# Optimization experiments

Hardware: AMD Instinct MI355X
Metric: run time of the kernel (lower is better)

## Reference

```python
import jax, jax.numpy as jnp
import numpy as np

B, IN, OUT, GD, TD, H, W, L = 16, 512, 256, 256, 256, 32, 32, 32
EPS_BN = 1e-5


def _conv2d(x, w, pad):
    return jax.lax.conv_general_dilated(
        x, w, window_strides=(1, 1), padding=[(pad, pad), (pad, pad)],
        dimension_numbers=("NCHW", "OIHW", "NCHW"))


def _up2(x):
    return jnp.repeat(jnp.repeat(x, 2, axis=2), 2, axis=3)


def _l2n(v):  # F.normalize(p=2, dim=1), eps=1e-12
    n = jnp.sqrt(jnp.sum(v * v, axis=1, keepdims=True))
    return v / jnp.maximum(n, 1e-12)


def _context(img_embs, words_embs, mask):
    i = _l2n(img_embs)            # [B, TD, P]
    wd = _l2n(words_embs)         # [B, TD, L]
    sim = jnp.einsum("bcp,bcl->bpl", i, wd)
    sim = jnp.where(mask[:, None, :], -jnp.inf, sim)
    attn = jax.nn.softmax(sim, axis=-1)
    return jnp.einsum("bpl,bcl->bcp", attn, wd)  # [B, TD, P]


def _bn(x, w, b):  # training-mode BatchNorm2d, biased variance
    m = jnp.mean(x, axis=(0, 2, 3), keepdims=True)
    v = jnp.var(x, axis=(0, 2, 3), keepdims=True)
    return (x - m) * jax.lax.rsqrt(v + EPS_BN) * w[None, :, None, None] + b[None, :, None, None]


def setup_inputs():
    key = jax.random.key(0)
    ks = jax.random.split(key, 16)
    s = 0.02
    COND = GD + TD
    return {
        "x": jax.random.normal(ks[0], (B, IN, H, W), jnp.float32),
        "global_cond": jax.random.normal(ks[1], (B, GD), jnp.float32),
        "words_embs": jax.random.normal(ks[2], (B, TD, L), jnp.float32),
        "mask": jax.random.randint(ks[3], (B, L), 0, 2).astype(bool),
        "w_img1": jax.random.normal(ks[4], (TD, IN), jnp.float32) * s,
        "w_img2": jax.random.normal(ks[5], (TD, OUT), jnp.float32) * s,
        "w_c1": jax.random.normal(ks[6], (OUT, IN, 3, 3), jnp.float32) * s,
        "w_c2": jax.random.normal(ks[7], (OUT, OUT, 3, 3), jnp.float32) * s,
        "bn1_w": jnp.ones((IN,), jnp.float32),
        "bn1_b": jnp.zeros((IN,), jnp.float32),
        "bn2_w": jnp.ones((OUT,), jnp.float32),
        "bn2_b": jnp.zeros((OUT,), jnp.float32),
        "w_g1": jax.random.normal(ks[8], (IN, COND), jnp.float32) * s,
        "b_g1": jnp.zeros((IN,), jnp.float32),
        "w_b1": jax.random.normal(ks[9], (IN, COND), jnp.float32) * s,
        "b_b1": jnp.zeros((IN,), jnp.float32),
        "w_g2": jax.random.normal(ks[10], (OUT, COND), jnp.float32) * s,
        "b_g2": jnp.zeros((OUT,), jnp.float32),
        "w_b2": jax.random.normal(ks[11], (OUT, COND), jnp.float32) * s,
        "b_b2": jnp.zeros((OUT,), jnp.float32),
        "w_sc": jax.random.normal(ks[12], (OUT, IN, 1, 1), jnp.float32) * s,
        "b_sc": jnp.zeros((OUT,), jnp.float32),
    }


def reference(x, global_cond, words_embs, mask,
              w_img1, w_img2, w_c1, w_c2,
              bn1_w, bn1_b, bn2_w, bn2_b,
              w_g1, b_g1, w_b1, b_b1,
              w_g2, b_g2, w_b2, b_b2,
              w_sc, b_sc):
    # ---- residual path, stage 1 ----
    img1 = jnp.einsum("tc,bcp->btp", w_img1, x.reshape(B, IN, H * W))
    ctx1 = _context(img1, words_embs, mask)                 # [B, TD, H*W]
    gc = jnp.broadcast_to(global_cond[:, :, None], (B, GD, H * W))
    cond1 = jnp.concatenate([gc, ctx1], axis=1)             # [B, GD+TD, H*W]
    gamma1 = jnp.einsum("oc,bcp->bop", w_g1, cond1) + b_g1[None, :, None]
    beta1 = jnp.einsum("oc,bcp->bop", w_b1, cond1) + b_b1[None, :, None]
    out = gamma1.reshape(B, IN, H, W) * _bn(x, bn1_w, bn1_b) + beta1.reshape(B, IN, H, W)
    out = jax.nn.relu(out)
    out = _up2(out)                                         # [B, IN, 2H, 2W]
    out = _conv2d(out, w_c1, 1)                             # [B, OUT, 2H, 2W]
    h2, w2 = 2 * H, 2 * W
    # ---- residual path, stage 2 ----
    img2 = jnp.einsum("tc,bcp->btp", w_img2, out.reshape(B, OUT, h2 * w2))
    ctx2 = _context(img2, words_embs, mask)                 # [B, TD, h2*w2]
    gc2 = jnp.broadcast_to(global_cond[:, :, None], (B, GD, h2 * w2))
    cond2 = jnp.concatenate([gc2, ctx2], axis=1)
    gamma2 = jnp.einsum("oc,bcp->bop", w_g2, cond2) + b_g2[None, :, None]
    beta2 = jnp.einsum("oc,bcp->bop", w_b2, cond2) + b_b2[None, :, None]
    out = gamma2.reshape(B, OUT, h2, w2) * _bn(out, bn2_w, bn2_b) + beta2.reshape(B, OUT, h2, w2)
    out = jax.nn.relu(out)
    out = _conv2d(out, w_c2, 1)
    # ---- shortcut ----
    sc = _conv2d(_up2(x), w_sc, 0) + b_sc[None, :, None, None]
    return out + sc
```

## Files before the change

kernel.cpp:

```cpp
#include <hip/hip_runtime.h>
#include <hip/hip_bf16.h>
#include <math.h>

#define NB 16
#define CIN1 512
#define COUT 256
#define GD 256
#define TD 256
#define LL 32
#define P1 1024
#define P2 4096
#define CONDC 512

typedef __attribute__((ext_vector_type(8))) short bf16x8;
typedef __attribute__((ext_vector_type(4))) float f32x4;
typedef unsigned short u16;

__device__ __forceinline__ u16 f2b(float f) {
  __hip_bfloat16 h = __float2bfloat16(f);
  return *(u16*)&h;
}

__global__ void bn_stats_kernel(const float* __restrict__ x, float* __restrict__ mean,
                                float* __restrict__ rstd, int C, int HW) {
  int c = blockIdx.x, t = threadIdx.x;
  float s = 0.f, sq = 0.f;
  for (int b = 0; b < NB; ++b) {
    const float* p = x + ((size_t)b * C + c) * HW;
    for (int i = t; i < HW; i += 256) { float v = p[i]; s += v; sq += v * v; }
  }
  __shared__ float ss[256], sq2[256];
  ss[t] = s; sq2[t] = sq; __syncthreads();
  for (int o = 128; o > 0; o >>= 1) {
    if (t < o) { ss[t] += ss[t + o]; sq2[t] += sq2[t + o]; }
    __syncthreads();
  }
  if (t == 0) {
    float n = (float)NB * (float)HW;
    float m = ss[0] / n;
    float v = sq2[0] / n - m * m;
    mean[c] = m;
    rstd[c] = rsqrtf(v + 1e-5f);
  }
}

__global__ void wdn_kernel(const float* __restrict__ we, float* __restrict__ wdn) {
  int b = blockIdx.x >> 5, l = blockIdx.x & 31;
  int t = threadIdx.x;
  const float* base = we + (size_t)b * TD * LL + l;
  float v[4]; float sq = 0.f;
#pragma unroll
  for (int k = 0; k < 4; ++k) { v[k] = base[(size_t)(t * 4 + k) * LL]; sq += v[k] * v[k]; }
#pragma unroll
  for (int o = 32; o > 0; o >>= 1) sq += __shfl_xor(sq, o);
  float r = 1.f / fmaxf(sqrtf(sq), 1e-12f);
  float* ob = wdn + (size_t)b * TD * LL + l;
#pragma unroll
  for (int k = 0; k < 4; ++k) ob[(size_t)(t * 4 + k) * LL] = v[k] * r;
}

__global__ void gvec_kernel(const float* __restrict__ Wg, const float* __restrict__ bias,
                            const float* __restrict__ gc, float* __restrict__ outv, int O) {
  int o = blockIdx.x * 64 + threadIdx.x;
  int b = blockIdx.y;
  if (o >= O) return;
  const float* wr = Wg + (size_t)o * CONDC;
  const float* g = gc + (size_t)b * GD;
  float s = 0.f;
  for (int c = 0; c < GD; ++c) s += wr[c] * g[c];
  outv[(size_t)b * O + o] = s + bias[o];
}

__global__ __launch_bounds__(256) void attnctx_kernel(
    const float* __restrict__ img, const float* __restrict__ wdn,
    const int* __restrict__ mask, float* __restrict__ ctx, int P) {
  __shared__ u16 imgT[64 * 72];
  __shared__ u16 wdnT[32 * 264];
  __shared__ u16 wdnC[256 * 40];
  __shared__ u16 attnB[64 * 40];
  __shared__ float sqP[4][64];
  __shared__ float rnL[64];
  const int b = blockIdx.y, p0 = blockIdx.x * 64;
  const int tid = threadIdx.x;
  const int w = tid >> 6, lane = tid & 63;
  const int l15 = lane & 15, lg = lane >> 4;
  const float* ib = img + (size_t)b * TD * P;
  const float* wb = wdn + (size_t)b * TD * LL;

  for (int i = tid; i < TD * LL; i += 256) {
    int t = i >> 5, l = i & 31;
    u16 v = f2b(wb[i]);
    wdnT[l * 264 + t] = v;
    wdnC[t * 40 + l] = v;
  }

  f32x4 s0 = {}, s1 = {};
  float ssq = 0.f;
  for (int q = 0; q < 4; ++q) {
#pragma unroll
    for (int i = 0; i < 16; i += 2) {
      int t = q * 64 + w * 16 + i;
      float v0 = ib[(size_t)t * P + p0 + lane];
      float v1 = ib[(size_t)(t + 1) * P + p0 + lane];
      ssq += v0 * v0 + v1 * v1;
      unsigned pk = (unsigned)f2b(v0) | ((unsigned)f2b(v1) << 16);
      *(unsigned*)(imgT + lane * 72 + w * 16 + i) = pk;
    }
    __syncthreads();
#pragma unroll
    for (int ks = 0; ks < 2; ++ks) {
      bf16x8 a = *(const bf16x8*)(imgT + (w * 16 + l15) * 72 + ks * 32 + lg * 8);
      bf16x8 b0 = *(const bf16x8*)(wdnT + l15 * 264 + q * 64 + ks * 32 + lg * 8);
      bf16x8 b1 = *(const bf16x8*)(wdnT + (16 + l15) * 264 + q * 64 + ks * 32 + lg * 8);
      s0 = __builtin_amdgcn_mfma_f32_16x16x32_bf16(a, b0, s0, 0, 0, 0);
      s1 = __builtin_amdgcn_mfma_f32_16x16x32_bf16(a, b1, s1, 0, 0, 0);
    }
    __syncthreads();
  }
  sqP[w][lane] = ssq;
  __syncthreads();
  if (tid < 64) {
    float s = sqP[0][tid] + sqP[1][tid] + sqP[2][tid] + sqP[3][tid];
    rnL[tid] = 1.f / fmaxf(sqrtf(s), 1e-12f);
  }
  __syncthreads();
  const bool m0 = mask[b * LL + l15] != 0;
  const bool m1 = mask[b * LL + 16 + l15] != 0;
#pragma unroll
  for (int k = 0; k < 4; ++k) {
    float rn = rnL[w * 16 + lg * 4 + k];
    float v0 = m0 ? -INFINITY : s0[k] * rn;
    float v1 = m1 ? -INFINITY : s1[k] * rn;
    float mx = fmaxf(v0, v1);
#pragma unroll
    for (int o = 1; o < 16; o <<= 1) mx = fmaxf(mx, __shfl_xor(mx, o));
    float e0 = expf(v0 - mx), e1 = expf(v1 - mx);
    float sm = e0 + e1;
#pragma unroll
    for (int o = 1; o < 16; o <<= 1) sm += __shfl_xor(sm, o);
    float inv = 1.f / sm;
    int px = w * 16 + lg * 4 + k;
    attnB[px * 40 + l15] = f2b(e0 * inv);
    attnB[px * 40 + 16 + l15] = f2b(e1 * inv);
  }
  __syncthreads();
  f32x4 acc[4][4] = {};
  bf16x8 bfr[4];
#pragma unroll
  for (int pt = 0; pt < 4; ++pt)
    bfr[pt] = *(const bf16x8*)(attnB + (pt * 16 + l15) * 40 + lg * 8);
#pragma unroll
  for (int cc = 0; cc < 4; ++cc) {
    bf16x8 a = *(const bf16x8*)(wdnC + ((w * 4 + cc) * 16 + l15) * 40 + lg * 8);
#pragma unroll
    for (int pt = 0; pt < 4; ++pt)
      acc[cc][pt] = __builtin_amdgcn_mfma_f32_16x16x32_bf16(a, bfr[pt], acc[cc][pt], 0, 0, 0);
  }
#pragma unroll
  for (int cc = 0; cc < 4; ++cc) {
#pragma unroll
    for (int pt = 0; pt < 4; ++pt) {
#pragma unroll
      for (int k = 0; k < 4; ++k) {
        int c = (w * 4 + cc) * 16 + lg * 4 + k;
        ctx[((size_t)b * TD + c) * P + p0 + pt * 16 + l15] = acc[cc][pt][k];
      }
    }
  }
}

__global__ __launch_bounds__(256, 2) void gemm_mfma_kernel(
    const float* __restrict__ W, int ldw, int c_off,
    const float* __restrict__ X, const float* __restrict__ vec,
    float* __restrict__ Y, int T, int C, int P) {
  __shared__ u16 Wl[2][128 * 44];
  __shared__ u16 Xl[2][128 * 40];
  const int b = blockIdx.z;
  const int t0 = blockIdx.y * 128, p0 = blockIdx.x * 128;
  const int tid = threadIdx.x;
  const int w = tid >> 6, lane = tid & 63;
  const int wo = w >> 1, wq = w & 1;
  const int l15 = lane & 15, lg = lane >> 4;
  const float* Xb = X + (size_t)b * C * P;
  const int wr = tid >> 1, wcH = tid & 1;
  const int xr = tid >> 3, xcG = tid & 7;
  const int csw = xr ^ ((xcG & 3) << 3);
  const float* wsrc = W + (size_t)(t0 + wr) * ldw + c_off + wcH * 16;
  const float* xsrc = Xb + (size_t)xr * P + p0 + xcG * 16;
  const int NK = C / 32;
  f32x4 acc[4][4] = {};
  float4 wreg[4], xreg[4];

#pragma unroll
  for (int j = 0; j < 4; ++j) {
    wreg[j] = *(const float4*)(wsrc + j * 4);
    xreg[j] = *(const float4*)(xsrc + j * 4);
  }
  {
    u16* dst = Wl[0] + wr * 44 + wcH * 16;
#pragma unroll
    for (int j = 0; j < 4; ++j) {
      *(ushort4*)(dst + j * 4) = make_ushort4(f2b(wreg[j].x), f2b(wreg[j].y), f2b(wreg[j].z), f2b(wreg[j].w));
      int px = xcG * 16 + j * 4;
      Xl[0][(px + 0) * 40 + csw] = f2b(xreg[j].x);
      Xl[0][(px + 1) * 40 + csw] = f2b(xreg[j].y);
      Xl[0][(px + 2) * 40 + csw] = f2b(xreg[j].z);
      Xl[0][(px + 3) * 40 + csw] = f2b(xreg[j].w);
    }
  }
  __syncthreads();

  for (int kb = 0; kb < NK; ++kb) {
    const int cur = kb & 1;
    if (kb + 1 < NK) {
      const int c0n = (kb + 1) * 32;
#pragma unroll
      for (int j = 0; j < 4; ++j) {
        wreg[j] = *(const float4*)(wsrc + c0n + j * 4);
        xreg[j] = *(const float4*)(xsrc + (size_t)c0n * P + j * 4);
      }
    }
    bf16x8 a[4], bb[4];
#pragma unroll
    for (int rr = 0; rr < 4; ++rr)
      a[rr] = *(const bf16x8*)(Wl[cur] + (wo * 64 + rr * 16 + l15) * 44 + lg * 8);
#pragma unroll
    for (int ss = 0; ss < 4; ++ss)
      bb[ss] = *(const bf16x8*)(Xl[cur] + (wq * 64 + ss * 16 + l15) * 40 + ((lg ^ ss) << 3));
#pragma unroll
    for (int rr = 0; rr < 4; ++rr)
#pragma unroll
      for (int ss = 0; ss < 4; ++ss)
        acc[rr][ss] = __builtin_amdgcn_mfma_f32_16x16x32_bf16(a[rr], bb[ss], acc[rr][ss], 0, 0, 0);
    if (kb + 1 < NK) {
      const int nxt = cur ^ 1;
      u16* dst = Wl[nxt] + wr * 44 + wcH * 16;
#pragma unroll
      for (int j = 0; j < 4; ++j) {
        *(ushort4*)(dst + j * 4) = make_ushort4(f2b(wreg[j].x), f2b(wreg[j].y), f2b(wreg[j].z), f2b(wreg[j].w));
        int px = xcG * 16 + j * 4;
        Xl[nxt][(px + 0) * 40 + csw] = f2b(xreg[j].x);
        Xl[nxt][(px + 1) * 40 + csw] = f2b(xreg[j].y);
        Xl[nxt][(px + 2) * 40 + csw] = f2b(xreg[j].z);
        Xl[nxt][(px + 3) * 40 + csw] = f2b(xreg[j].w);
      }
      __syncthreads();
    }
  }
#pragma unroll
  for (int rr = 0; rr < 4; ++rr) {
    int tb = t0 + wo * 64 + rr * 16 + lg * 4;
#pragma unroll
    for (int ss = 0; ss < 4; ++ss) {
      int p = p0 + wq * 64 + ss * 16 + l15;
#pragma unroll
      for (int k = 0; k < 4; ++k) {
        int t = tb + k;
        float val = acc[rr][ss][k];
        if (vec) val += vec[(size_t)b * T + t];
        Y[((size_t)b * T + t) * P + p] = val;
      }
    }
  }
}

__global__ __launch_bounds__(256, 2) void gbact_kernel(
    const float* __restrict__ Wg, const float* __restrict__ Wb,
    const float* __restrict__ ctx, const float* __restrict__ gvec,
    const float* __restrict__ bvec, const float* __restrict__ xin,
    const float* __restrict__ mean, const float* __restrict__ rstd,
    const float* __restrict__ bnw, const float* __restrict__ bnb,
    u16* __restrict__ outb, int C, int P) {
  __shared__ u16 shmem[2][16384];
  const int b = blockIdx.z, t0 = blockIdx.y * 128, p0 = blockIdx.x * 128;
  const int tid = threadIdx.x;
  const int w = tid >> 6, lane = tid & 63;
  const int wo = w >> 1, wq = w & 1;
  const int l15 = lane & 15, lg = lane >> 4;
  const float* Xb = ctx + (size_t)b * TD * P;
  const int wr = tid >> 1, wcH = tid & 1;
  const int xr = tid >> 3, xcG = tid & 7;
  const int csw = xr ^ ((xcG & 3) << 3);
  const float* gsrc = Wg + (size_t)(t0 + wr) * CONDC + GD + wcH * 16;
  const float* bsrc = Wb + (size_t)(t0 + wr) * CONDC + GD + wcH * 16;
  const float* xsrc = Xb + (size_t)xr * P + p0 + xcG * 16;
  const int NK = TD / 32;
  f32x4 accg[4][4] = {}, accb[4][4] = {};
  float4 greg[4], breg[4], xreg[4];

#pragma unroll
  for (int j = 0; j < 4; ++j) {
    greg[j] = *(const float4*)(gsrc + j * 4);
    breg[j] = *(const float4*)(bsrc + j * 4);
    xreg[j] = *(const float4*)(xsrc + j * 4);
  }
  {
    u16* dg = shmem[0] + wr * 44 + wcH * 16;
    u16* db = shmem[0] + 5632 + wr * 44 + wcH * 16;
    u16* xl = shmem[0] + 11264;
#pragma unroll
    for (int j = 0; j < 4; ++j) {
      *(ushort4*)(dg + j * 4) = make_ushort4(f2b(greg[j].x), f2b(greg[j].y), f2b(greg[j].z), f2b(greg[j].w));
      *(ushort4*)(db + j * 4) = make_ushort4(f2b(breg[j].x), f2b(breg[j].y), f2b(breg[j].z), f2b(breg[j].w));
      int px = xcG * 16 + j * 4;
      xl[(px + 0) * 40 + csw] = f2b(xreg[j].x);
      xl[(px + 1) * 40 + csw] = f2b(xreg[j].y);
      xl[(px + 2) * 40 + csw] = f2b(xreg[j].z);
      xl[(px + 3) * 40 + csw] = f2b(xreg[j].w);
    }
  }
  __syncthreads();

  for (int kb = 0; kb < NK; ++kb) {
    const int cur = kb & 1;
    if (kb + 1 < NK) {
      const int c0n = (kb + 1) * 32;
#pragma unroll
      for (int j = 0; j < 4; ++j) {
        greg[j] = *(const float4*)(gsrc + c0n + j * 4);
        breg[j] = *(const float4*)(bsrc + c0n + j * 4);
        xreg[j] = *(const float4*)(xsrc + (size_t)c0n * P + j * 4);
      }
    }
    bf16x8 ag[4], ab[4], bb[4];
#pragma unroll
    for (int rr = 0; rr < 4; ++rr) {
      ag[rr] = *(const bf16x8*)(shmem[cur] + (wo * 64 + rr * 16 + l15) * 44 + lg * 8);
      ab[rr] = *(const bf16x8*)(shmem[cur] + 5632 + (wo * 64 + rr * 16 + l15) * 44 + lg * 8);
    }
#pragma unroll
    for (int ss = 0; ss < 4; ++ss)
      bb[ss] = *(const bf16x8*)(shmem[cur] + 11264 + (wq * 64 + ss * 16 + l15) * 40 + ((lg ^ ss) << 3));
#pragma unroll
    for (int rr = 0; rr < 4; ++rr)
#pragma unroll
      for (int ss = 0; ss < 4; ++ss) {
        accg[rr][ss] = __builtin_amdgcn_mfma_f32_16x16x32_bf16(ag[rr], bb[ss], accg[rr][ss], 0, 0, 0);
        accb[rr][ss] = __builtin_amdgcn_mfma_f32_16x16x32_bf16(ab[rr], bb[ss], accb[rr][ss], 0, 0, 0);
      }
    if (kb + 1 < NK) {
      const int nxt = cur ^ 1;
      u16* dg = shmem[nxt] + wr * 44 + wcH * 16;
      u16* db = shmem[nxt] + 5632 + wr * 44 + wcH * 16;
      u16* xl = shmem[nxt] + 11264;
#pragma unroll
      for (int j = 0; j < 4; ++j) {
        *(ushort4*)(dg + j * 4) = make_ushort4(f2b(greg[j].x), f2b(greg[j].y), f2b(greg[j].z), f2b(greg[j].w));
        *(ushort4*)(db + j * 4) = make_ushort4(f2b(breg[j].x), f2b(breg[j].y), f2b(breg[j].z), f2b(breg[j].w));
        int px = xcG * 16 + j * 4;
        xl[(px + 0) * 40 + csw] = f2b(xreg[j].x);
        xl[(px + 1) * 40 + csw] = f2b(xreg[j].y);
        xl[(px + 2) * 40 + csw] = f2b(xreg[j].z);
        xl[(px + 3) * 40 + csw] = f2b(xreg[j].w);
      }
      __syncthreads();
    }
  }
  __syncthreads();
  u16* tbuf = &shmem[0][0];
#pragma unroll
  for (int rr = 0; rr < 4; ++rr) {
    float gv[4], bv[4], mm[4], rs[4], bB[4];
#pragma unroll
    for (int k = 0; k < 4; ++k) {
      int c = t0 + wo * 64 + rr * 16 + lg * 4 + k;
      gv[k] = gvec[(size_t)b * C + c];
      bv[k] = bvec[(size_t)b * C + c];
      mm[k] = mean[c]; rs[k] = rstd[c] * bnw[c]; bB[k] = bnb[c];
    }
#pragma unroll
    for (int ss = 0; ss < 4; ++ss) {
#pragma unroll
      for (int k = 0; k < 4; ++k) {
        int cl = wo * 64 + rr * 16 + lg * 4 + k;
        int pl = wq * 64 + ss * 16 + l15;
        float xv = xin[((size_t)b * C + t0 + cl) * P + p0 + pl];
        float g = accg[rr][ss][k] + gv[k];
        float be = accb[rr][ss][k] + bv[k];
        float val = fmaxf(g * ((xv - mm[k]) * rs[k] + bB[k]) + be, 0.f);
        tbuf[pl * 136 + cl] = f2b(val);
      }
    }
  }
  __syncthreads();
  const int pr = tid >> 1, h = tid & 1;
#pragma unroll
  for (int j = 0; j < 8; ++j) {
    uint4 v = *(uint4*)(tbuf + pr * 136 + h * 64 + j * 8);
    *(uint4*)(outb + ((size_t)b * P + p0 + pr) * C + t0 + h * 64 + j * 8) = v;
  }
}

__global__ void pack_w_kernel(const float* __restrict__ w, u16* __restrict__ wp, int O, int CIN) {
  int lin = blockIdx.x * 256 + threadIdx.x;
  if (lin >= O * CIN) return;
  int o = lin / CIN, c = lin - o * CIN;
  int c0blk = c >> 5, lg = (c >> 3) & 3, cc = c & 7;
  int ot = o >> 4, l15 = o & 15;
  int lane = lg * 16 + l15;
  size_t base = (((size_t)c0blk * (O >> 4) + ot) * 64 + lane) * 8 + cc;
  size_t posStride = (size_t)(CIN >> 5) * (O >> 4) * 512;
  const float* src = w + (size_t)lin * 9;
#pragma unroll
  for (int pos = 0; pos < 9; ++pos)
    wp[pos * posStride + base] = f2b(src[pos]);
}

template <int CIN, bool UP>
__global__ __launch_bounds__(256, 2) void conv_mfma_kernel(
    const u16* __restrict__ Wp, const u16* __restrict__ Xt,
    const float* __restrict__ scs, const float* __restrict__ scb,
    float* __restrict__ Y) {
  constexpr int S = UP ? 32 : 64;
  constexpr int NC0 = CIN >> 5;
  __shared__ u16 Xs[2][4 * 66 * 36];
  const int b = blockIdx.z, pxT = blockIdx.x;
  const int tid = threadIdx.x;
  const int w = tid >> 6, lane = tid & 63;
  const int wo = w >> 1, wp_ = w & 1;
  const int l15 = lane & 15, lg = lane >> 4;
  const int Y0 = pxT * 2;
  const u16* Xb = Xt + (size_t)b * S * S * CIN;
  const size_t posStride = (size_t)NC0 * 16 * 512;
  f32x4 acc[8][4] = {};
  uint2 st[9];

#pragma unroll
  for (int j = 0; j < 9; ++j) {
    int i = tid + j * 256;
    if (i < 2112) {
      int r = i / 528, rem = i - r * 528, col = rem >> 3, ch = rem & 7;
      int uy = Y0 - 1 + r, ux = col - 1;
      uint2 v = make_uint2(0u, 0u);
      if (uy >= 0 && uy < 64 && ux >= 0 && ux < 64) {
        int sy = UP ? (uy >> 1) : uy, sx = UP ? (ux >> 1) : ux;
        v = *(const uint2*)(Xb + ((size_t)sy * S + sx) * CIN + ch * 4);
      }
      st[j] = v;
    }
  }
#pragma unroll
  for (int j = 0; j < 9; ++j) {
    int i = tid + j * 256;
    if (i < 2112) {
      int r = i / 528, rem = i - r * 528, col = rem >> 3, ch = rem & 7;
      *(uint2*)(&Xs[0][(r * 66 + col) * 36 + ch * 4]) = st[j];
    }
  }
  __syncthreads();

  for (int c0b = 0; c0b < NC0; ++c0b) {
    const int cur = c0b & 1;
    if (c0b + 1 < NC0) {
      const int c0n = (c0b + 1) << 5;
#pragma unroll
      for (int j = 0; j < 9; ++j) {
        int i = tid + j * 256;
        if (i < 2112) {
          int r = i / 528, rem = i - r * 528, col = rem >> 3, ch = rem & 7;
          int uy = Y0 - 1 + r, ux = col - 1;
          uint2 v = make_uint2(0u, 0u);
          if (uy >= 0 && uy < 64 && ux >= 0 && ux < 64) {
            int sy = UP ? (uy >> 1) : uy, sx = UP ? (ux >> 1) : ux;
            v = *(const uint2*)(Xb + ((size_t)sy * S + sx) * CIN + c0n + ch * 4);
          }
          st[j] = v;
        }
      }
    }
    {
      const u16* wbB = Wp + ((size_t)c0b * 16 + wo * 8) * 512 + lane * 8;
      bf16x8 aC[8], aN[8];
#pragma unroll
      for (int rr = 0; rr < 8; ++rr)
        aC[rr] = *(const bf16x8*)(wbB + rr * 512);
#pragma unroll
      for (int pos = 0; pos < 9; ++pos) {
        const int ky = pos / 3, kx = pos - ky * 3;
        if (pos < 8) {
          const u16* wbn = wbB + (size_t)(pos + 1) * posStride;
#pragma unroll
          for (int rr = 0; rr < 8; ++rr)
            aN[rr] = *(const bf16x8*)(wbn + rr * 512);
        }
        const int rowb = ((wp_ + ky) * 66 + kx) * 36 + lg * 8;
#pragma unroll
        for (int ss = 0; ss < 4; ++ss) {
          int idx = rowb + (ss * 16 + l15) * 36;
          union { uint2 q[2]; bf16x8 v; } u;
          u.q[0] = *(const uint2*)(&Xs[cur][idx]);
          u.q[1] = *(const uint2*)(&Xs[cur][idx + 4]);
#pragma unroll
          for (int rr = 0; rr < 8; ++rr)
            acc[rr][ss] = __builtin_amdgcn_mfma_f32_16x16x32_bf16(aC[rr], u.v, acc[rr][ss], 0, 0, 0);
        }
#pragma unroll
        for (int rr = 0; rr < 8; ++rr) aC[rr] = aN[rr];
      }
    }
    if (c0b + 1 < NC0) {
#pragma unroll
      for (int j = 0; j < 9; ++j) {
        int i = tid + j * 256;
        if (i < 2112) {
          int r = i / 528, rem = i - r * 528, col = rem >> 3, ch = rem & 7;
          *(uint2*)(&Xs[cur ^ 1][(r * 66 + col) * 36 + ch * 4]) = st[j];
        }
      }
      __syncthreads();
    }
  }
  const int oBase = wo * 128 + lg * 4;
  const int pxBase = pxT * 128 + wp_ * 64 + l15;
#pragma unroll
  for (int rr = 0; rr < 8; ++rr) {
#pragma unroll
    for (int ss = 0; ss < 4; ++ss) {
      int px = pxBase + ss * 16;
#pragma unroll
      for (int k = 0; k < 4; ++k) {
        int o = oBase + rr * 16 + k;
        float val = acc[rr][ss][k];
        if (scs) {
          int gx = px & 63;
          val += scs[((size_t)b * COUT + o) * P1 + pxT * 32 + (gx >> 1)] + scb[o];
        }
        Y[((size_t)b * COUT + o) * 4096 + px] = val;
      }
    }
  }
}

extern "C" void kernel_launch(void* const* d_in, const int* in_sizes, int n_in,
                              void* d_out, int out_size, void* d_ws, size_t ws_size,
                              hipStream_t stream) {
  const float* x      = (const float*)d_in[0];
  const float* gcond  = (const float*)d_in[1];
  const float* wemb   = (const float*)d_in[2];
  const int*   mask   = (const int*)d_in[3];
  const float* w_img1 = (const float*)d_in[4];
  const float* w_img2 = (const float*)d_in[5];
  const float* w_c1   = (const float*)d_in[6];
  const float* w_c2   = (const float*)d_in[7];
  const float* bn1_w  = (const float*)d_in[8];
  const float* bn1_b  = (const float*)d_in[9];
  const float* bn2_w  = (const float*)d_in[10];
  const float* bn2_b  = (const float*)d_in[11];
  const float* w_g1   = (const float*)d_in[12];
  const float* b_g1   = (const float*)d_in[13];
  const float* w_b1   = (const float*)d_in[14];
  const float* b_b1   = (const float*)d_in[15];
  const float* w_g2   = (const float*)d_in[16];
  const float* b_g2   = (const float*)d_in[17];
  const float* w_b2   = (const float*)d_in[18];
  const float* b_b2   = (const float*)d_in[19];
  const float* w_sc   = (const float*)d_in[20];
  const float* b_sc   = (const float*)d_in[21];
  float* out = (float*)d_out;
  float* ws = (float*)d_ws;

  const size_t MF = 16777216;
  float* A  = ws;
  float* Br = ws + MF;
  float* Cr = ws + 2 * MF;
  float* SM = ws + 3 * MF;
  float* wdn   = SM;
  float* mean1 = SM + 131072;
  float* rstd1 = mean1 + 512;
  float* mean2 = rstd1 + 512;
  float* rstd2 = mean2 + 256;
  float* gvec1 = rstd2 + 256;
  float* bvec1 = gvec1 + 8192;
  float* gvec2 = bvec1 + 8192;
  float* bvec2 = gvec2 + 4096;
  float* wsp   = bvec2 + 4096;
  u16* Wp1 = (u16*)wsp;
  u16* Wp2 = (u16*)(wsp + 655360);

  float* img1   = A;
  float* ctx1   = A + 4194304;
  u16*   Xt1    = (u16*)(A + 8388608);
  float* conv1o = Cr;
  float* img2   = Br;
  float* ctx2   = A;
  u16*   Xt2    = (u16*)Br;
  float* scs    = Cr;

  bn_stats_kernel<<<dim3(CIN1), dim3(256), 0, stream>>>(x, mean1, rstd1, CIN1, P1);
  wdn_kernel<<<dim3(NB * LL), dim3(64), 0, stream>>>(wemb, wdn);
  pack_w_kernel<<<dim3(COUT * CIN1 / 256), dim3(256), 0, stream>>>(w_c1, Wp1, COUT, CIN1);
  pack_w_kernel<<<dim3(COUT * COUT / 256), dim3(256), 0, stream>>>(w_c2, Wp2, COUT, COUT);
  gemm_mfma_kernel<<<dim3(P1 / 128, TD / 128, NB), dim3(256), 0, stream>>>(
      w_img1, CIN1, 0, x, nullptr, img1, TD, CIN1, P1);
  attnctx_kernel<<<dim3(P1 / 64, NB), dim3(256), 0, stream>>>(img1, wdn, mask, ctx1, P1);
  gvec_kernel<<<dim3(CIN1 / 64, NB), dim3(64), 0, stream>>>(w_g1, b_g1, gcond, gvec1, CIN1);
  gvec_kernel<<<dim3(CIN1 / 64, NB), dim3(64), 0, stream>>>(w_b1, b_b1, gcond, bvec1, CIN1);
  gbact_kernel<<<dim3(P1 / 128, CIN1 / 128, NB), dim3(256), 0, stream>>>(
      w_g1, w_b1, ctx1, gvec1, bvec1, x, mean1, rstd1, bn1_w, bn1_b, Xt1, CIN1, P1);
  conv_mfma_kernel<CIN1, true><<<dim3(32, 1, NB), dim3(256), 0, stream>>>(
      Wp1, Xt1, nullptr, nullptr, conv1o);

  bn_stats_kernel<<<dim3(COUT), dim3(256), 0, stream>>>(conv1o, mean2, rstd2, COUT, P2);
  gemm_mfma_kernel<<<dim3(P2 / 128, TD / 128, NB), dim3(256), 0, stream>>>(
      w_img2, COUT, 0, conv1o, nullptr, img2, TD, COUT, P2);
  attnctx_kernel<<<dim3(P2 / 64, NB), dim3(256), 0, stream>>>(img2, wdn, mask, ctx2, P2);
  gvec_kernel<<<dim3(COUT / 64, NB), dim3(64), 0, stream>>>(w_g2, b_g2, gcond, gvec2, COUT);
  gvec_kernel<<<dim3(COUT / 64, NB), dim3(64), 0, stream>>>(w_b2, b_b2, gcond, bvec2, COUT);
  gbact_kernel<<<dim3(P2 / 128, COUT / 128, NB), dim3(256), 0, stream>>>(
      w_g2, w_b2, ctx2, gvec2, bvec2, conv1o, mean2, rstd2, bn2_w, bn2_b, Xt2, COUT, P2);
  gemm_mfma_kernel<<<dim3(P1 / 128, COUT / 128, NB), dim3(256), 0, stream>>>(
      w_sc, CIN1, 0, x, nullptr, scs, COUT, CIN1, P1);
  conv_mfma_kernel<COUT, false><<<dim3(32, 1, NB), dim3(256), 0, stream>>>(
      Wp2, Xt2, scs, b_sc, out);
}
```

Measured before the change: 546.4 us.

## Store intermediate activations (img, ctx, conv1 output) in bf16 instead of fp32

The intermediate tensors between kernels (image projections, attention context, first conv output) are now written and read as bf16 rather than fp32. GEMM, attention, gamma/beta and BN-stats kernels are templated to accept bf16 inputs and outputs. The aim is to roughly halve global memory traffic for these large 16x256x4096 buffers and to skip redundant fp32-to-bf16 conversions, since the MFMA paths already consume bf16. In exchange, BN statistics and the elementwise affine now read a rounded conv1 output, which adds precision loss.

```diff
diff --git a/kernel.cpp b/kernel.cpp
--- a/kernel.cpp
+++ b/kernel.cpp
@@ -20,14 +20,24 @@
   __hip_bfloat16 h = __float2bfloat16(f);
   return *(u16*)&h;
 }
-
-__global__ void bn_stats_kernel(const float* __restrict__ x, float* __restrict__ mean,
+__device__ __forceinline__ float b2f(u16 v) {
+  unsigned u = ((unsigned)v) << 16;
+  float f;
+  __builtin_memcpy(&f, &u, 4);
+  return f;
+}
+
+template <bool BF>
+__global__ void bn_stats_kernel(const void* xv, float* __restrict__ mean,
                                 float* __restrict__ rstd, int C, int HW) {
   int c = blockIdx.x, t = threadIdx.x;
   float s = 0.f, sq = 0.f;
   for (int b = 0; b < NB; ++b) {
-    const float* p = x + ((size_t)b * C + c) * HW;
-    for (int i = t; i < HW; i += 256) { float v = p[i]; s += v; sq += v * v; }
+    size_t base = ((size_t)b * C + c) * HW;
+    for (int i = t; i < HW; i += 256) {
+      float v = BF ? b2f(((const u16*)xv)[base + i]) : ((const float*)xv)[base + i];
+      s += v; sq += v * v;
+    }
   }
   __shared__ float ss[256], sq2[256];
   ss[t] = s; sq2[t] = sq; __syncthreads();
@@ -72,8 +82,8 @@
 }
 
 __global__ __launch_bounds__(256) void attnctx_kernel(
-    const float* __restrict__ img, const float* __restrict__ wdn,
-    const int* __restrict__ mask, float* __restrict__ ctx, int P) {
+    const u16* __restrict__ img, const float* __restrict__ wdn,
+    const int* __restrict__ mask, u16* __restrict__ ctx, int P) {
   __shared__ u16 imgT[64 * 72];
   __shared__ u16 wdnT[32 * 264];
   __shared__ u16 wdnC[256 * 40];
@@ -84,7 +94,7 @@
   const int tid = threadIdx.x;
   const int w = tid >> 6, lane = tid & 63;
   const int l15 = lane & 15, lg = lane >> 4;
-  const float* ib = img + (size_t)b * TD * P;
+  const u16* ib = img + (size_t)b * TD * P;
   const float* wb = wdn + (size_t)b * TD * LL;
 
   for (int i = tid; i < TD * LL; i += 256) {
@@ -100,10 +110,11 @@
 #pragma unroll
     for (int i = 0; i < 16; i += 2) {
       int t = q * 64 + w * 16 + i;
-      float v0 = ib[(size_t)t * P + p0 + lane];
-      float v1 = ib[(size_t)(t + 1) * P + p0 + lane];
+      u16 h0 = ib[(size_t)t * P + p0 + lane];
+      u16 h1 = ib[(size_t)(t + 1) * P + p0 + lane];
+      float v0 = b2f(h0), v1 = b2f(h1);
       ssq += v0 * v0 + v1 * v1;
-      unsigned pk = (unsigned)f2b(v0) | ((unsigned)f2b(v1) << 16);
+      unsigned pk = (unsigned)h0 | ((unsigned)h1 << 16);
       *(unsigned*)(imgT + lane * 72 + w * 16 + i) = pk;
     }
     __syncthreads();
@@ -163,16 +174,17 @@
 #pragma unroll
       for (int k = 0; k < 4; ++k) {
         int c = (w * 4 + cc) * 16 + lg * 4 + k;
-        ctx[((size_t)b * TD + c) * P + p0 + pt * 16 + l15] = acc[cc][pt][k];
-      }
-    }
-  }
-}
-
+        ctx[((size_t)b * TD + c) * P + p0 + pt * 16 + l15] = f2b(acc[cc][pt][k]);
+      }
+    }
+  }
+}
+
+template <bool XB, bool YB>
 __global__ __launch_bounds__(256, 2) void gemm_mfma_kernel(
     const float* __restrict__ W, int ldw, int c_off,
-    const float* __restrict__ X, const float* __restrict__ vec,
-    float* __restrict__ Y, int T, int C, int P) {
+    const void* __restrict__ Xv, const float* __restrict__ vec,
+    void* __restrict__ Yv, int T, int C, int P) {
   __shared__ u16 Wl[2][128 * 44];
   __shared__ u16 Xl[2][128 * 40];
   const int b = blockIdx.z;
@@ -181,32 +193,41 @@
   const int w = tid >> 6, lane = tid & 63;
   const int wo = w >> 1, wq = w & 1;
   const int l15 = lane & 15, lg = lane >> 4;
-  const float* Xb = X + (size_t)b * C * P;
   const int wr = tid >> 1, wcH = tid & 1;
   const int xr = tid >> 3, xcG = tid & 7;
   const int csw = xr ^ ((xcG & 3) << 3);
   const float* wsrc = W + (size_t)(t0 + wr) * ldw + c_off + wcH * 16;
-  const float* xsrc = Xb + (size_t)xr * P + p0 + xcG * 16;
+  const float* xsrc32 = XB ? nullptr : (const float*)Xv + (size_t)b * C * P + (size_t)xr * P + p0 + xcG * 16;
+  const u16* xsrc16 = XB ? (const u16*)Xv + (size_t)b * C * P + (size_t)xr * P + p0 + xcG * 16 : nullptr;
   const int NK = C / 32;
   f32x4 acc[4][4] = {};
-  float4 wreg[4], xreg[4];
-
-#pragma unroll
-  for (int j = 0; j < 4; ++j) {
-    wreg[j] = *(const float4*)(wsrc + j * 4);
-    xreg[j] = *(const float4*)(xsrc + j * 4);
+  float4 wreg[4];
+  u16 xst[16];
+
+#pragma unroll
+  for (int j = 0; j < 4; ++j) wreg[j] = *(const float4*)(wsrc + j * 4);
+  if (XB) {
+    union { u16 u[16]; uint4 q[2]; } xu;
+    xu.q[0] = *(const uint4*)(xsrc16);
+    xu.q[1] = *(const uint4*)(xsrc16 + 8);
+#pragma unroll
+    for (int i = 0; i < 16; ++i) xst[i] = xu.u[i];
+  } else {
+#pragma unroll
+    for (int j = 0; j < 4; ++j) {
+      float4 v = *(const float4*)(xsrc32 + j * 4);
+      xst[j * 4 + 0] = f2b(v.x); xst[j * 4 + 1] = f2b(v.y);
+      xst[j * 4 + 2] = f2b(v.z); xst[j * 4 + 3] = f2b(v.w);
+    }
   }
   {
     u16* dst = Wl[0] + wr * 44 + wcH * 16;
 #pragma unroll
-    for (int j = 0; j < 4; ++j) {
+    for (int j = 0; j < 4; ++j)
       *(ushort4*)(dst + j * 4) = make_ushort4(f2b(wreg[j].x), f2b(wreg[j].y), f2b(wreg[j].z), f2b(wreg[j].w));
-      int px = xcG * 16 + j * 4;
-      Xl[0][(px + 0) * 40 + csw] = f2b(xreg[j].x);
-      Xl[0][(px + 1) * 40 + csw] = f2b(xreg[j].y);
-      Xl[0][(px + 2) * 40 + csw] = f2b(xreg[j].z);
-      Xl[0][(px + 3) * 40 + csw] = f2b(xreg[j].w);
-    }
+#pragma unroll
+    for (int i = 0; i < 16; ++i)
+      Xl[0][(xcG * 16 + i) * 40 + csw] = xst[i];
   }
   __syncthreads();
 
@@ -215,9 +236,20 @@
     if (kb + 1 < NK) {
       const int c0n = (kb + 1) * 32;
 #pragma unroll
-      for (int j = 0; j < 4; ++j) {
-        wreg[j] = *(const float4*)(wsrc + c0n + j * 4);
-        xreg[j] = *(const float4*)(xsrc + (size_t)c0n * P + j * 4);
+      for (int j = 0; j < 4; ++j) wreg[j] = *(const float4*)(wsrc + c0n + j * 4);
+      if (XB) {
+        union { u16 u[16]; uint4 q[2]; } xu;
+        xu.q[0] = *(const uint4*)(xsrc16 + (size_t)c0n * P);
+        xu.q[1] = *(const uint4*)(xsrc16 + (size_t)c0n * P + 8);
+#pragma unroll
+        for (int i = 0; i < 16; ++i) xst[i] = xu.u[i];
+      } else {
+#pragma unroll
+        for (int j = 0; j < 4; ++j) {
+          float4 v = *(const float4*)(xsrc32 + (size_t)c0n * P + j * 4);
+          xst[j * 4 + 0] = f2b(v.x); xst[j * 4 + 1] = f2b(v.y);
+          xst[j * 4 + 2] = f2b(v.z); xst[j * 4 + 3] = f2b(v.w);
+        }
       }
     }
     bf16x8 a[4], bb[4];
@@ -236,14 +268,11 @@
       const int nxt = cur ^ 1;
       u16* dst = Wl[nxt] + wr * 44 + wcH * 16;
 #pragma unroll
-      for (int j = 0; j < 4; ++j) {
+      for (int j = 0; j < 4; ++j)
         *(ushort4*)(dst + j * 4) = make_ushort4(f2b(wreg[j].x), f2b(wreg[j].y), f2b(wreg[j].z), f2b(wreg[j].w));
-        int px = xcG * 16 + j * 4;
-        Xl[nxt][(px + 0) * 40 + csw] = f2b(xreg[j].x);
-        Xl[nxt][(px + 1) * 40 + csw] = f2b(xreg[j].y);
-        Xl[nxt][(px + 2) * 40 + csw] = f2b(xreg[j].z);
-        Xl[nxt][(px + 3) * 40 + csw] = f2b(xreg[j].w);
-      }
+#pragma unroll
+      for (int i = 0; i < 16; ++i)
+        Xl[nxt][(xcG * 16 + i) * 40 + csw] = xst[i];
       __syncthreads();
     }
   }
@@ -258,16 +287,18 @@
         int t = tb + k;
         float val = acc[rr][ss][k];
         if (vec) val += vec[(size_t)b * T + t];
-        Y[((size_t)b * T + t) * P + p] = val;
-      }
-    }
-  }
-}
-
+        if (YB) ((u16*)Yv)[((size_t)b * T + t) * P + p] = f2b(val);
+        else    ((float*)Yv)[((size_t)b * T + t) * P + p] = val;
+      }
+    }
+  }
+}
+
+template <bool XINB>
 __global__ __launch_bounds__(256, 2) void gbact_kernel(
     const float* __restrict__ Wg, const float* __restrict__ Wb,
-    const float* __restrict__ ctx, const float* __restrict__ gvec,
-    const float* __restrict__ bvec, const float* __restrict__ xin,
+    const u16* __restrict__ ctx, const float* __restrict__ gvec,
+    const float* __restrict__ bvec, const void* __restrict__ xinv,
     const float* __restrict__ mean, const float* __restrict__ rstd,
     const float* __restrict__ bnw, const float* __restrict__ bnb,
     u16* __restrict__ outb, int C, int P) {
@@ -277,22 +308,28 @@
   const int w = tid >> 6, lane = tid & 63;
   const int wo = w >> 1, wq = w & 1;
   const int l15 = lane & 15, lg = lane >> 4;
-  const float* Xb = ctx + (size_t)b * TD * P;
   const int wr = tid >> 1, wcH = tid & 1;
   const int xr = tid >> 3, xcG = tid & 7;
   const int csw = xr ^ ((xcG & 3) << 3);
   const float* gsrc = Wg + (size_t)(t0 + wr) * CONDC + GD + wcH * 16;
   const float* bsrc = Wb + (size_t)(t0 + wr) * CONDC + GD + wcH * 16;
-  const float* xsrc = Xb + (size_t)xr * P + p0 + xcG * 16;
+  const u16* xsrc = ctx + (size_t)b * TD * P + (size_t)xr * P + p0 + xcG * 16;
   const int NK = TD / 32;
   f32x4 accg[4][4] = {}, accb[4][4] = {};
-  float4 greg[4], breg[4], xreg[4];
+  float4 greg[4], breg[4];
+  u16 xst[16];
 
 #pragma unroll
   for (int j = 0; j < 4; ++j) {
     greg[j] = *(const float4*)(gsrc + j * 4);
     breg[j] = *(const float4*)(bsrc + j * 4);
-    xreg[j] = *(const float4*)(xsrc + j * 4);
+  }
+  {
+    union { u16 u[16]; uint4 q[2]; } xu;
+    xu.q[0] = *(const uint4*)(xsrc);
+    xu.q[1] = *(const uint4*)(xsrc + 8);
+#pragma unroll
+    for (int i = 0; i < 16; ++i) xst[i] = xu.u[i];
   }
   {
     u16* dg = shmem[0] + wr * 44 + wcH * 16;
@@ -302,12 +339,10 @@
     for (int j = 0; j < 4; ++j) {
       *(ushort4*)(dg + j * 4) = make_ushort4(f2b(greg[j].x), f2b(greg[j].y), f2b(greg[j].z), f2b(greg[j].w));
       *(ushort4*)(db + j * 4) = make_ushort4(f2b(breg[j].x), f2b(breg[j].y), f2b(breg[j].z), f2b(breg[j].w));
-      int px = xcG * 16 + j * 4;
-      xl[(px + 0) * 40 + csw] = f2b(xreg[j].x);
-      xl[(px + 1) * 40 + csw] = f2b(xreg[j].y);
-      xl[(px + 2) * 40 + csw] = f2b(xreg[j].z);
-      xl[(px + 3) * 40 + csw] = f2b(xreg[j].w);
-    }
+    }
+#pragma unroll
+    for (int i = 0; i < 16; ++i)
+      xl[(xcG * 16 + i) * 40 + csw] = xst[i];
   }
   __syncthreads();
 
@@ -319,8 +354,12 @@
       for (int j = 0; j < 4; ++j) {
         greg[j] = *(const float4*)(gsrc + c0n + j * 4);
         breg[j] = *(const float4*)(bsrc + c0n + j * 4);
-        xreg[j] = *(const float4*)(xsrc + (size_t)c0n * P + j * 4);
-      }
+      }
+      union { u16 u[16]; uint4 q[2]; } xu;
+      xu.q[0] = *(const uint4*)(xsrc + (size_t)c0n * P);
+      xu.q[1] = *(const uint4*)(xsrc + (size_t)c0n * P + 8);
+#pragma unroll
+      for (int i = 0; i < 16; ++i) xst[i] = xu.u[i];
     }
     bf16x8 ag[4], ab[4], bb[4];
 #pragma unroll
@@ -347,12 +386,10 @@
       for (int j = 0; j < 4; ++j) {
         *(ushort4*)(dg + j * 4) = make_ushort4(f2b(greg[j].x), f2b(greg[j].y), f2b(greg[j].z), f2b(greg[j].w));
         *(ushort4*)(db + j * 4) = make_ushort4(f2b(breg[j].x), f2b(breg[j].y), f2b(breg[j].z), f2b(breg[j].w));
-        int px = xcG * 16 + j * 4;
-        xl[(px + 0) * 40 + csw] = f2b(xreg[j].x);
-        xl[(px + 1) * 40 + csw] = f2b(xreg[j].y);
-        xl[(px + 2) * 40 + csw] = f2b(xreg[j].z);
-        xl[(px + 3) * 40 + csw] = f2b(xreg[j].w);
-      }
+      }
+#pragma unroll
+      for (int i = 0; i < 16; ++i)
+        xl[(xcG * 16 + i) * 40 + csw] = xst[i];
       __syncthreads();
     }
   }
@@ -374,7 +411,8 @@
       for (int k = 0; k < 4; ++k) {
         int cl = wo * 64 + rr * 16 + lg * 4 + k;
         int pl = wq * 64 + ss * 16 + l15;
-        float xv = xin[((size_t)b * C + t0 + cl) * P + p0 + pl];
+        size_t xidx = ((size_t)b * C + t0 + cl) * P + p0 + pl;
+        float xv = XINB ? b2f(((const u16*)xinv)[xidx]) : ((const float*)xinv)[xidx];
         float g = accg[rr][ss][k] + gv[k];
         float be = accb[rr][ss][k] + bv[k];
         float val = fmaxf(g * ((xv - mm[k]) * rs[k] + bB[k]) + be, 0.f);
@@ -406,11 +444,11 @@
     wp[pos * posStride + base] = f2b(src[pos]);
 }
 
-template <int CIN, bool UP>
+template <int CIN, bool UP, bool OUTB>
 __global__ __launch_bounds__(256, 2) void conv_mfma_kernel(
     const u16* __restrict__ Wp, const u16* __restrict__ Xt,
     const float* __restrict__ scs, const float* __restrict__ scb,
-    float* __restrict__ Y) {
+    void* __restrict__ Yv) {
   constexpr int S = UP ? 32 : 64;
   constexpr int NC0 = CIN >> 5;
   __shared__ u16 Xs[2][4 * 66 * 36];
@@ -525,7 +563,8 @@
           int gx = px & 63;
           val += scs[((size_t)b * COUT + o) * P1 + pxT * 32 + (gx >> 1)] + scb[o];
         }
-        Y[((size_t)b * COUT + o) * 4096 + px] = val;
+        if (OUTB) ((u16*)Yv)[((size_t)b * COUT + o) * 4096 + px] = f2b(val);
+        else      ((float*)Yv)[((size_t)b * COUT + o) * 4096 + px] = val;
       }
     }
   }
@@ -577,39 +616,39 @@
   u16* Wp1 = (u16*)wsp;
   u16* Wp2 = (u16*)(wsp + 655360);
 
-  float* img1   = A;
-  float* ctx1   = A + 4194304;
-  u16*   Xt1    = (u16*)(A + 8388608);
-  float* conv1o = Cr;
-  float* img2   = Br;
-  float* ctx2   = A;
-  u16*   Xt2    = (u16*)Br;
-  float* scs    = Cr;
-
-  bn_stats_kernel<<<dim3(CIN1), dim3(256), 0, stream>>>(x, mean1, rstd1, CIN1, P1);
+  u16* img1   = (u16*)A;
+  u16* ctx1   = (u16*)A + 4194304;
+  u16* Xt1    = (u16*)A + 8388608;
+  u16* conv1o = (u16*)Cr;
+  u16* img2   = (u16*)Br;
+  u16* ctx2   = (u16*)A;
+  u16* Xt2    = (u16*)Br;
+  float* scs  = Cr;
+
+  bn_stats_kernel<false><<<dim3(CIN1), dim3(256), 0, stream>>>(x, mean1, rstd1, CIN1, P1);
   wdn_kernel<<<dim3(NB * LL), dim3(64), 0, stream>>>(wemb, wdn);
   pack_w_kernel<<<dim3(COUT * CIN1 / 256), dim3(256), 0, stream>>>(w_c1, Wp1, COUT, CIN1);
   pack_w_kernel<<<dim3(COUT * COUT / 256), dim3(256), 0, stream>>>(w_c2, Wp2, COUT, COUT);
-  gemm_mfma_kernel<<<dim3(P1 / 128, TD / 128, NB), dim3(256), 0, stream>>>(
+  gemm_mfma_kernel<false, true><<<dim3(P1 / 128, TD / 128, NB), dim3(256), 0, stream>>>(
       w_img1, CIN1, 0, x, nullptr, img1, TD, CIN1, P1);
   attnctx_kernel<<<dim3(P1 / 64, NB), dim3(256), 0, stream>>>(img1, wdn, mask, ctx1, P1);
   gvec_kernel<<<dim3(CIN1 / 64, NB), dim3(64), 0, stream>>>(w_g1, b_g1, gcond, gvec1, CIN1);
   gvec_kernel<<<dim3(CIN1 / 64, NB), dim3(64), 0, stream>>>(w_b1, b_b1, gcond, bvec1, CIN1);
-  gbact_kernel<<<dim3(P1 / 128, CIN1 / 128, NB), dim3(256), 0, stream>>>(
+  gbact_kernel<false><<<dim3(P1 / 128, CIN1 / 128, NB), dim3(256), 0, stream>>>(
       w_g1, w_b1, ctx1, gvec1, bvec1, x, mean1, rstd1, bn1_w, bn1_b, Xt1, CIN1, P1);
-  conv_mfma_kernel<CIN1, true><<<dim3(32, 1, NB), dim3(256), 0, stream>>>(
+  conv_mfma_kernel<CIN1, true, true><<<dim3(32, 1, NB), dim3(256), 0, stream>>>(
       Wp1, Xt1, nullptr, nullptr, conv1o);
 
-  bn_stats_kernel<<<dim3(COUT), dim3(256), 0, stream>>>(conv1o, mean2, rstd2, COUT, P2);
-  gemm_mfma_kernel<<<dim3(P2 / 128, TD / 128, NB), dim3(256), 0, stream>>>(
+  bn_stats_kernel<true><<<dim3(COUT), dim3(256), 0, stream>>>(conv1o, mean2, rstd2, COUT, P2);
+  gemm_mfma_kernel<true, true><<<dim3(P2 / 128, TD / 128, NB), dim3(256), 0, stream>>>(
       w_img2, COUT, 0, conv1o, nullptr, img2, TD, COUT, P2);
   attnctx_kernel<<<dim3(P2 / 64, NB), dim3(256), 0, stream>>>(img2, wdn, mask, ctx2, P2);
   gvec_kernel<<<dim3(COUT / 64, NB), dim3(64), 0, stream>>>(w_g2, b_g2, gcond, gvec2, COUT);
   gvec_kernel<<<dim3(COUT / 64, NB), dim3(64), 0, stream>>>(w_b2, b_b2, gcond, bvec2, COUT);
-  gbact_kernel<<<dim3(P2 / 128, COUT / 128, NB), dim3(256), 0, stream>>>(
+  gbact_kernel<true><<<dim3(P2 / 128, COUT / 128, NB), dim3(256), 0, stream>>>(
       w_g2, w_b2, ctx2, gvec2, bvec2, conv1o, mean2, rstd2, bn2_w, bn2_b, Xt2, COUT, P2);
-  gemm_mfma_kernel<<<dim3(P1 / 128, COUT / 128, NB), dim3(256), 0, stream>>>(
+  gemm_mfma_kernel<false, false><<<dim3(P1 / 128, COUT / 128, NB), dim3(256), 0, stream>>>(
       w_sc, CIN1, 0, x, nullptr, scs, COUT, CIN1, P1);
-  conv_mfma_kernel<COUT, false><<<dim3(32, 1, NB), dim3(256), 0, stream>>>(
+  conv_mfma_kernel<COUT, false, false><<<dim3(32, 1, NB), dim3(256), 0, stream>>>(
       Wp2, Xt2, scs, b_sc, out);
 }
```

Result: faster. 502.0 us (-8.1%).
